# Optimization experiments

Measured on AMD Instinct MI355X. Metric: run time of the kernel, lower is better.

Reference implementation:

```python
import jax, jax.numpy as jnp
import numpy as np

HEADS = 16
DIM_HEAD = 64
SCALE = DIM_HEAD ** -0.5


def setup_inputs() -> dict:
    key = jax.random.key(0)
    k1, k2, k3, k4 = jax.random.split(key, 4)
    b, n, dim = 2, 2048, 1024
    inner = HEADS * DIM_HEAD  # 1024
    x = jax.random.normal(k1, (b, n, dim), dtype=jnp.float32)
    mask = jax.random.randint(k2, (b, n), 0, 2, dtype=jnp.int32)
    Wqkv = jax.random.normal(k3, (dim, inner), dtype=jnp.float32) * (dim ** -0.5)
    Wout = jax.random.normal(k4, (inner, dim), dtype=jnp.float32) * (inner ** -0.5)
    bout = jnp.zeros((dim,), dtype=jnp.float32)
    return {"x": x, "mask": mask, "Wqkv": Wqkv, "Wout": Wout, "bout": bout}


def reference(x, mask, Wqkv, Wout, bout):
    b, n, _ = x.shape
    # shared projection: w acts as q = k = v (CRATE subspace attention)
    w = jnp.einsum('bnd,de->bne', x, Wqkv)
    w = w.reshape(b, n, HEADS, DIM_HEAD).transpose(0, 2, 1, 3)  # b h n d
    dots = jnp.einsum('bhid,bhjd->bhij', w, w) * SCALE           # b h n n
    attn = jax.nn.softmax(dots, axis=-1)
    # post-softmax multiplicative masking (mask=1 zeros the column)
    m = mask[:, None, None, :].astype(attn.dtype)
    attn = attn * (1.0 - m)
    out = jnp.einsum('bhij,bhjd->bhid', attn, w)                 # b h n d
    out = out.transpose(0, 2, 1, 3).reshape(b, n, HEADS * DIM_HEAD)
    return jnp.einsum('bne,ed->bnd', out, Wout) + bout
```

## Files before the change

### kernel.cpp

```cpp
#include <hip/hip_runtime.h>
#include <hip/hip_bf16.h>
#include <stdint.h>

typedef unsigned short u16;
typedef unsigned int u32;
typedef __bf16 bf16x8 __attribute__((ext_vector_type(8)));
typedef float f32x4 __attribute__((ext_vector_type(4)));

#define AS1 __attribute__((address_space(1)))
#define AS3 __attribute__((address_space(3)))

__device__ __forceinline__ void async16(const u16* g, u16* l) {
  __builtin_amdgcn_global_load_lds((const AS1 uint32_t*)(const void*)g,
                                   (AS3 uint32_t*)l, 16, 0, 0);
}

__device__ __forceinline__ u16 f2bf(float v) {
  union { __hip_bfloat16 b; u16 u; } c; c.b = __float2bfloat16(v); return c.u;
}

__device__ __forceinline__ uint4 pack8(float4 lo, float4 hi) {
  uint4 q;
  q.x = (u32)f2bf(lo.x) | ((u32)f2bf(lo.y) << 16);
  q.y = (u32)f2bf(lo.z) | ((u32)f2bf(lo.w) << 16);
  q.z = (u32)f2bf(hi.x) | ((u32)f2bf(hi.y) << 16);
  q.w = (u32)f2bf(hi.z) | ((u32)f2bf(hi.w) << 16);
  return q;
}

__global__ void cvt_x(const float* __restrict__ in, u16* __restrict__ out) {
  int i = (blockIdx.x * 256 + threadIdx.x) * 8;
  float4 lo = *(const float4*)(in + i);
  float4 hi = *(const float4*)(in + i + 4);
  *(uint4*)(out + i) = pack8(lo, hi);
}

__global__ void transpose1024_cvt2(const float* __restrict__ in0, u16* __restrict__ out0,
                                   const float* __restrict__ in1, u16* __restrict__ out1) {
  const float* in = blockIdx.z ? in1 : in0;
  u16* out = blockIdx.z ? out1 : out0;
  __shared__ u16 tile[32][33];
  int tx = threadIdx.x, ty = threadIdx.y;
  int c0 = blockIdx.x * 32, r0 = blockIdx.y * 32;
#pragma unroll
  for (int i = 0; i < 32; i += 8)
    tile[ty + i][tx] = f2bf(in[(size_t)(r0 + ty + i) * 1024 + c0 + tx]);
  __syncthreads();
#pragma unroll
  for (int i = 0; i < 32; i += 8)
    out[(size_t)(c0 + ty + i) * 1024 + r0 + tx] = tile[tx][ty + i];
}

__global__ void scale_transpose_v(const u16* __restrict__ w, const int* __restrict__ mask,
                                  u16* __restrict__ Vt) {
  __shared__ u16 tile[32][33];
  const int tx = threadIdx.x, ty = threadIdx.y;
  const int j0 = blockIdx.x * 32, d0 = blockIdx.y * 32;
  const int bh = blockIdx.z, b = bh >> 4, hc = (bh & 15) * 64;
#pragma unroll
  for (int i = 0; i < 32; i += 8) {
    int j = j0 + ty + i;
    u16 v = w[(size_t)(b * 2048 + j) * 1024 + hc + d0 + tx];
    tile[ty + i][tx] = mask[b * 2048 + j] ? (u16)0 : v;
  }
  __syncthreads();
#pragma unroll
  for (int i = 0; i < 32; i += 8)
    Vt[((size_t)bh * 64 + d0 + ty + i) * 2048 + j0 + tx] = tile[tx][ty + i];
}

template<bool OUT_F32>
__launch_bounds__(256)
__global__ void gemm_bt(const u16* __restrict__ A, const u16* __restrict__ BT,
                        void* __restrict__ Cp, const float* __restrict__ bias,
                        int M, int N, int K) {
  __shared__ __align__(16) u16 As[2][128 * 32];
  __shared__ __align__(16) u16 Bs[2][64 * 32];
  const int t = threadIdx.x;
  const int lane = t & 63, wave = t >> 6;
  const int m0 = blockIdx.x * 128, n0 = blockIdx.y * 64;
  const int wm = (wave & 1) * 64, wn = (wave >> 1) * 32;
  const int lrow = lane & 15, quad = lane >> 4;

  f32x4 acc[4][2] = {};

  const int ar = t >> 2, ac = (t & 3) * 8;
  const u16* gA = A + (size_t)(m0 + ar) * K + ac;
  const u16* gB = BT + (size_t)(n0 + ar) * K + ac;

  for (int k0 = 0; k0 < K; k0 += 64) {
    async16(gA + k0,                       &As[0][t * 8]);
    async16(gA + k0 + (size_t)64 * K,      &As[0][t * 8 + 2048]);
    async16(gA + k0 + 32,                  &As[1][t * 8]);
    async16(gA + k0 + 32 + (size_t)64 * K, &As[1][t * 8 + 2048]);
    async16(gB + k0,                       &Bs[0][t * 8]);
    async16(gB + k0 + 32,                  &Bs[1][t * 8]);
    __syncthreads();

#pragma unroll
    for (int kk = 0; kk < 2; kk++) {
      bf16x8 af[4], bfr[2];
#pragma unroll
      for (int i = 0; i < 4; i++)
        af[i] = *(const bf16x8*)&As[kk][(wm + i * 16 + lrow) * 32 + quad * 8];
#pragma unroll
      for (int j = 0; j < 2; j++)
        bfr[j] = *(const bf16x8*)&Bs[kk][(wn + j * 16 + lrow) * 32 + quad * 8];
#pragma unroll
      for (int i = 0; i < 4; i++)
#pragma unroll
        for (int j = 0; j < 2; j++)
          acc[i][j] = __builtin_amdgcn_mfma_f32_16x16x32_bf16(af[i], bfr[j], acc[i][j], 0, 0, 0);
    }
    __syncthreads();
  }

  float bv[2];
#pragma unroll
  for (int j = 0; j < 2; j++)
    bv[j] = bias ? bias[n0 + wn + j * 16 + lrow] : 0.f;

#pragma unroll
  for (int i = 0; i < 4; i++) {
#pragma unroll
    for (int r = 0; r < 4; r++) {
      int row = m0 + wm + i * 16 + quad * 4 + r;
#pragma unroll
      for (int j = 0; j < 2; j++) {
        size_t ci = (size_t)row * N + n0 + wn + j * 16 + lrow;
        float v = acc[i][j][r] + bv[j];
        if (OUT_F32) ((float*)Cp)[ci] = v;
        else ((u16*)Cp)[ci] = f2bf(v);
      }
    }
  }
}

#define SV 72
#define C1 0.18033688f
#define C2 -28.853901f
__launch_bounds__(256)
__global__ void attn_kernel(const u16* __restrict__ w, const u16* __restrict__ Vt,
                            u16* __restrict__ y) {
  __shared__ __align__(16) u16 Ws[64 * SV];
  __shared__ __align__(16) u16 VTs[64 * SV];
  __shared__ __align__(16) u16 P[4][16 * SV];
  const int t = threadIdx.x, lane = t & 63, wave = t >> 6;
  const int lrow = lane & 15, quad = lane >> 4;
  const int bh = blockIdx.y, b = bh >> 4, h = bh & 15;
  const int q0 = blockIdx.x * 64;
  const size_t rowb = (size_t)b * 2048;
  const int hc = h * 64;
  u16* Pw = P[wave];

  const int sr = t >> 2, sc = (t & 3) * 16;
  const u16* kg = &w[(rowb + sr) * 1024 + hc + sc];
  const u16* vg = &Vt[((size_t)bh * 64 + sr) * 2048 + sc];

  bf16x8 qf0, qf1;
  {
    const size_t qrow = rowb + q0 + wave * 16 + lrow;
    qf0 = *(const bf16x8*)&w[qrow * 1024 + hc + quad * 8];
    qf1 = *(const bf16x8*)&w[qrow * 1024 + hc + 32 + quad * 8];
  }

  uint4 ka = *(const uint4*)kg, kb = *(const uint4*)(kg + 8);
  uint4 va = *(const uint4*)vg, vc = *(const uint4*)(vg + 8);

  f32x4 o[4] = {};
  float lrun[4] = {0.f, 0.f, 0.f, 0.f};

  for (int j0 = 0; j0 < 2048; j0 += 64) {
    __syncthreads();
    *(uint4*)&Ws[sr * SV + sc]      = ka;
    *(uint4*)&Ws[sr * SV + sc + 8]  = kb;
    *(uint4*)&VTs[sr * SV + sc]     = va;
    *(uint4*)&VTs[sr * SV + sc + 8] = vc;
    __syncthreads();

    if (j0 + 64 < 2048) {
      const u16* kn = kg + (size_t)(j0 + 64) * 1024;
      const u16* vn = vg + j0 + 64;
      ka = *(const uint4*)kn; kb = *(const uint4*)(kn + 8);
      va = *(const uint4*)vn; vc = *(const uint4*)(vn + 8);
    }

    f32x4 st[4];
#pragma unroll
    for (int jt = 0; jt < 4; jt++) {
      bf16x8 kf0 = *(const bf16x8*)&Ws[(jt * 16 + lrow) * SV + quad * 8];
      bf16x8 kf1 = *(const bf16x8*)&Ws[(jt * 16 + lrow) * SV + 32 + quad * 8];
      f32x4 z = {};
      z = __builtin_amdgcn_mfma_f32_16x16x32_bf16(qf0, kf0, z, 0, 0, 0);
      z = __builtin_amdgcn_mfma_f32_16x16x32_bf16(qf1, kf1, z, 0, 0, 0);
      st[jt] = z;
    }

#pragma unroll
    for (int jt = 0; jt < 4; jt++) {
#pragma unroll
      for (int r = 0; r < 4; r++) {
        float e = exp2f(fmaf(st[jt][r], C1, C2));
        lrun[r] += e;
        Pw[(quad * 4 + r) * SV + jt * 16 + lrow] = f2bf(e);
      }
    }

    bf16x8 pa0 = *(const bf16x8*)&Pw[lrow * SV + quad * 8];
    bf16x8 pa1 = *(const bf16x8*)&Pw[lrow * SV + 32 + quad * 8];
#pragma unroll
    for (int dt = 0; dt < 4; dt++) {
      bf16x8 vb0 = *(const bf16x8*)&VTs[(dt * 16 + lrow) * SV + quad * 8];
      bf16x8 vb1 = *(const bf16x8*)&VTs[(dt * 16 + lrow) * SV + 32 + quad * 8];
      o[dt] = __builtin_amdgcn_mfma_f32_16x16x32_bf16(pa0, vb0, o[dt], 0, 0, 0);
      o[dt] = __builtin_amdgcn_mfma_f32_16x16x32_bf16(pa1, vb1, o[dt], 0, 0, 0);
    }
  }

#pragma unroll
  for (int r = 0; r < 4; r++) {
    float l = lrun[r];
#pragma unroll
    for (int s = 8; s >= 1; s >>= 1)
      l += __shfl_xor(l, s, 64);
    float inv = 1.f / l;
    const size_t orow = rowb + q0 + wave * 16 + quad * 4 + r;
#pragma unroll
    for (int dt = 0; dt < 4; dt++)
      y[orow * 1024 + hc + dt * 16 + lrow] = f2bf(o[dt][r] * inv);
  }
}

extern "C" void kernel_launch(void* const* d_in, const int* in_sizes, int n_in,
                              void* d_out, int out_size, void* d_ws, size_t ws_size,
                              hipStream_t stream) {
  const float* x    = (const float*)d_in[0];
  const int* mask   = (const int*)d_in[1];
  const float* Wqkv = (const float*)d_in[2];
  const float* Wout = (const float*)d_in[3];
  const float* bout = (const float*)d_in[4];
  float* out = (float*)d_out;

  u16* w     = (u16*)d_ws;
  u16* y     = w + 4096 * 1024;
  u16* WqkvT = y + 4096 * 1024;
  u16* WoutT = WqkvT + 1024 * 1024;
  u16* Vt    = WoutT + 1024 * 1024;
  u16* xb    = y;

  cvt_x<<<2048, 256, 0, stream>>>(x, xb);
  transpose1024_cvt2<<<dim3(32, 32, 2), dim3(32, 8), 0, stream>>>(Wqkv, WqkvT, Wout, WoutT);
  gemm_bt<false><<<dim3(32, 16), 256, 0, stream>>>(xb, WqkvT, w, nullptr, 4096, 1024, 1024);
  scale_transpose_v<<<dim3(64, 2, 32), dim3(32, 8), 0, stream>>>(w, mask, Vt);
  attn_kernel<<<dim3(32, 32), 256, 0, stream>>>(w, Vt, y);
  gemm_bt<true><<<dim3(32, 16), 256, 0, stream>>>(y, WoutT, out, bout, 4096, 1024, 1024);
}
```

Baseline: 193.6 us.

## Fuse V mask-transpose into QKV GEMM epilogue, merge prep kernels, double-buffer GEMMs

Folds the x conversion and both weight transposes into a single prep launch. The masked V transpose is moved into the first GEMM's epilogue, staged through shared memory, so the separate scale_transpose_v kernel and its re-read of w go away. Both GEMMs now double-buffer their shared-memory tiles so the next K-slice load overlaps the current MFMA work. This cuts launches and global traffic, at the cost of twice the LDS per GEMM block, which may lower occupancy.

```diff
diff --git a/kernel.cpp b/kernel.cpp
--- a/kernel.cpp
+++ b/kernel.cpp
@@ -1,6 +1,7 @@
 #include <hip/hip_runtime.h>
 #include <hip/hip_bf16.h>
 #include <stdint.h>
+
 
 typedef unsigned short u16;
 typedef unsigned int u32;
@@ -28,17 +29,21 @@
   return q;
 }
 
-__global__ void cvt_x(const float* __restrict__ in, u16* __restrict__ out) {
-  int i = (blockIdx.x * 256 + threadIdx.x) * 8;
-  float4 lo = *(const float4*)(in + i);
-  float4 hi = *(const float4*)(in + i + 4);
-  *(uint4*)(out + i) = pack8(lo, hi);
-}
-
-__global__ void transpose1024_cvt2(const float* __restrict__ in0, u16* __restrict__ out0,
-                                   const float* __restrict__ in1, u16* __restrict__ out1) {
-  const float* in = blockIdx.z ? in1 : in0;
-  u16* out = blockIdx.z ? out1 : out0;
+__global__ void prep(const float* __restrict__ Wqkv, u16* __restrict__ WqkvT,
+                     const float* __restrict__ Wout, u16* __restrict__ WoutT,
+                     const float* __restrict__ x, u16* __restrict__ xb) {
+  const int z = blockIdx.z;
+  if (z >= 2) {
+    int bid = blockIdx.y * 32 + blockIdx.x;
+    size_t i = (((size_t)(z - 2) * 1024 + bid) * 256
+                + threadIdx.y * 32 + threadIdx.x) * 8;
+    float4 lo = *(const float4*)(x + i);
+    float4 hi = *(const float4*)(x + i + 4);
+    *(uint4*)(xb + i) = pack8(lo, hi);
+    return;
+  }
+  const float* in = z ? Wout : Wqkv;
+  u16* out = z ? WoutT : WqkvT;
   __shared__ u16 tile[32][33];
   int tx = threadIdx.x, ty = threadIdx.y;
   int c0 = blockIdx.x * 32, r0 = blockIdx.y * 32;
@@ -51,31 +56,13 @@
     out[(size_t)(c0 + ty + i) * 1024 + r0 + tx] = tile[tx][ty + i];
 }
 
-__global__ void scale_transpose_v(const u16* __restrict__ w, const int* __restrict__ mask,
-                                  u16* __restrict__ Vt) {
-  __shared__ u16 tile[32][33];
-  const int tx = threadIdx.x, ty = threadIdx.y;
-  const int j0 = blockIdx.x * 32, d0 = blockIdx.y * 32;
-  const int bh = blockIdx.z, b = bh >> 4, hc = (bh & 15) * 64;
-#pragma unroll
-  for (int i = 0; i < 32; i += 8) {
-    int j = j0 + ty + i;
-    u16 v = w[(size_t)(b * 2048 + j) * 1024 + hc + d0 + tx];
-    tile[ty + i][tx] = mask[b * 2048 + j] ? (u16)0 : v;
-  }
-  __syncthreads();
-#pragma unroll
-  for (int i = 0; i < 32; i += 8)
-    Vt[((size_t)bh * 64 + d0 + ty + i) * 2048 + j0 + tx] = tile[tx][ty + i];
-}
-
-template<bool OUT_F32>
 __launch_bounds__(256)
-__global__ void gemm_bt(const u16* __restrict__ A, const u16* __restrict__ BT,
-                        void* __restrict__ Cp, const float* __restrict__ bias,
-                        int M, int N, int K) {
-  __shared__ __align__(16) u16 As[2][128 * 32];
-  __shared__ __align__(16) u16 Bs[2][64 * 32];
+__global__ void gemm1_fused(const u16* __restrict__ A, const u16* __restrict__ BT,
+                            u16* __restrict__ w, const int* __restrict__ mask,
+                            u16* __restrict__ Vt) {
+  const int K = 1024, N = 1024;
+  __shared__ __align__(16) u16 As[2][2][128 * 32];
+  __shared__ __align__(16) u16 Bs[2][2][64 * 32];
   const int t = threadIdx.x;
   const int lane = t & 63, wave = t >> 6;
   const int m0 = blockIdx.x * 128, n0 = blockIdx.y * 64;
@@ -88,24 +75,30 @@
   const u16* gA = A + (size_t)(m0 + ar) * K + ac;
   const u16* gB = BT + (size_t)(n0 + ar) * K + ac;
 
+#define STAGE1(buf, k0)                                              \
+  do {                                                               \
+    async16(gA + (k0),                       &As[buf][0][t * 8]);    \
+    async16(gA + (k0) + (size_t)64 * K,      &As[buf][0][t * 8 + 2048]); \
+    async16(gA + (k0) + 32,                  &As[buf][1][t * 8]);    \
+    async16(gA + (k0) + 32 + (size_t)64 * K, &As[buf][1][t * 8 + 2048]); \
+    async16(gB + (k0),                       &Bs[buf][0][t * 8]);    \
+    async16(gB + (k0) + 32,                  &Bs[buf][1][t * 8]);    \
+  } while (0)
+
+  STAGE1(0, 0);
+  __syncthreads();
+  int p = 0;
   for (int k0 = 0; k0 < K; k0 += 64) {
-    async16(gA + k0,                       &As[0][t * 8]);
-    async16(gA + k0 + (size_t)64 * K,      &As[0][t * 8 + 2048]);
-    async16(gA + k0 + 32,                  &As[1][t * 8]);
-    async16(gA + k0 + 32 + (size_t)64 * K, &As[1][t * 8 + 2048]);
-    async16(gB + k0,                       &Bs[0][t * 8]);
-    async16(gB + k0 + 32,                  &Bs[1][t * 8]);
-    __syncthreads();
-
+    if (k0 + 64 < K) STAGE1(p ^ 1, k0 + 64);
 #pragma unroll
     for (int kk = 0; kk < 2; kk++) {
       bf16x8 af[4], bfr[2];
 #pragma unroll
       for (int i = 0; i < 4; i++)
-        af[i] = *(const bf16x8*)&As[kk][(wm + i * 16 + lrow) * 32 + quad * 8];
+        af[i] = *(const bf16x8*)&As[p][kk][(wm + i * 16 + lrow) * 32 + quad * 8];
 #pragma unroll
       for (int j = 0; j < 2; j++)
-        bfr[j] = *(const bf16x8*)&Bs[kk][(wn + j * 16 + lrow) * 32 + quad * 8];
+        bfr[j] = *(const bf16x8*)&Bs[p][kk][(wn + j * 16 + lrow) * 32 + quad * 8];
 #pragma unroll
       for (int i = 0; i < 4; i++)
 #pragma unroll
@@ -113,27 +106,108 @@
           acc[i][j] = __builtin_amdgcn_mfma_f32_16x16x32_bf16(af[i], bfr[j], acc[i][j], 0, 0, 0);
     }
     __syncthreads();
+    p ^= 1;
+  }
+
+  u16* T = &As[0][0][0];
+#pragma unroll
+  for (int i = 0; i < 4; i++) {
+    int4 mk = *(const int4*)&mask[m0 + wm + i * 16 + quad * 4];
+    int mkk[4] = {mk.x, mk.y, mk.z, mk.w};
+#pragma unroll
+    for (int j2 = 0; j2 < 2; j2++) {
+      union { u16 s[4]; double d; } pk;
+#pragma unroll
+      for (int r = 0; r < 4; r++) {
+        int row = wm + i * 16 + quad * 4 + r;
+        u16 v = f2bf(acc[i][j2][r]);
+        w[(size_t)(m0 + row) * N + n0 + wn + j2 * 16 + lrow] = v;
+        pk.s[r] = mkk[r] ? (u16)0 : v;
+      }
+      int col = wn + j2 * 16 + lrow;
+      *(double*)&T[col * 136 + wm + i * 16 + quad * 4] = pk.d;
+    }
+  }
+  __syncthreads();
+  {
+    const int bq = m0 >> 11, jl0 = m0 & 2047, h = n0 >> 6;
+    u16* vt = Vt + ((size_t)(bq * 16 + h) * 64) * 2048 + jl0;
+    const int dd = t >> 2, cc = (t & 3) * 32;
+#pragma unroll
+    for (int c = 0; c < 4; c++) {
+      uint4 q = *(const uint4*)&T[dd * 136 + cc + c * 8];
+      *(uint4*)&vt[(size_t)dd * 2048 + cc + c * 8] = q;
+    }
+  }
+#undef STAGE1
+}
+
+__launch_bounds__(256)
+__global__ void gemm2(const u16* __restrict__ A, const u16* __restrict__ BT,
+                      float* __restrict__ C, const float* __restrict__ bias) {
+  const int K = 1024, N = 1024;
+  __shared__ __align__(16) u16 As[2][2][128 * 32];
+  __shared__ __align__(16) u16 Bs[2][2][64 * 32];
+  const int t = threadIdx.x;
+  const int lane = t & 63, wave = t >> 6;
+  const int m0 = blockIdx.x * 128, n0 = blockIdx.y * 64;
+  const int wm = (wave & 1) * 64, wn = (wave >> 1) * 32;
+  const int lrow = lane & 15, quad = lane >> 4;
+
+  f32x4 acc[4][2] = {};
+
+  const int ar = t >> 2, ac = (t & 3) * 8;
+  const u16* gA = A + (size_t)(m0 + ar) * K + ac;
+  const u16* gB = BT + (size_t)(n0 + ar) * K + ac;
+
+#define STAGE2(buf, k0)                                              \
+  do {                                                               \
+    async16(gA + (k0),                       &As[buf][0][t * 8]);    \
+    async16(gA + (k0) + (size_t)64 * K,      &As[buf][0][t * 8 + 2048]); \
+    async16(gA + (k0) + 32,                  &As[buf][1][t * 8]);    \
+    async16(gA + (k0) + 32 + (size_t)64 * K, &As[buf][1][t * 8 + 2048]); \
+    async16(gB + (k0),                       &Bs[buf][0][t * 8]);    \
+    async16(gB + (k0) + 32,                  &Bs[buf][1][t * 8]);    \
+  } while (0)
+
+  STAGE2(0, 0);
+  __syncthreads();
+  int p = 0;
+  for (int k0 = 0; k0 < K; k0 += 64) {
+    if (k0 + 64 < K) STAGE2(p ^ 1, k0 + 64);
+#pragma unroll
+    for (int kk = 0; kk < 2; kk++) {
+      bf16x8 af[4], bfr[2];
+#pragma unroll
+      for (int i = 0; i < 4; i++)
+        af[i] = *(const bf16x8*)&As[p][kk][(wm + i * 16 + lrow) * 32 + quad * 8];
+#pragma unroll
+      for (int j = 0; j < 2; j++)
+        bfr[j] = *(const bf16x8*)&Bs[p][kk][(wn + j * 16 + lrow) * 32 + quad * 8];
+#pragma unroll
+      for (int i = 0; i < 4; i++)
+#pragma unroll
+        for (int j = 0; j < 2; j++)
+          acc[i][j] = __builtin_amdgcn_mfma_f32_16x16x32_bf16(af[i], bfr[j], acc[i][j], 0, 0, 0);
+    }
+    __syncthreads();
+    p ^= 1;
   }
 
   float bv[2];
 #pragma unroll
   for (int j = 0; j < 2; j++)
-    bv[j] = bias ? bias[n0 + wn + j * 16 + lrow] : 0.f;
-
-#pragma unroll
-  for (int i = 0; i < 4; i++) {
+    bv[j] = bias[n0 + wn + j * 16 + lrow];
+#pragma unroll
+  for (int i = 0; i < 4; i++)
 #pragma unroll
     for (int r = 0; r < 4; r++) {
       int row = m0 + wm + i * 16 + quad * 4 + r;
 #pragma unroll
-      for (int j = 0; j < 2; j++) {
-        size_t ci = (size_t)row * N + n0 + wn + j * 16 + lrow;
-        float v = acc[i][j][r] + bv[j];
-        if (OUT_F32) ((float*)Cp)[ci] = v;
-        else ((u16*)Cp)[ci] = f2bf(v);
-      }
-    }
-  }
+      for (int j = 0; j < 2; j++)
+        C[(size_t)row * N + n0 + wn + j * 16 + lrow] = acc[i][j][r] + bv[j];
+    }
+#undef STAGE2
 }
 
 #define SV 72
@@ -248,10 +322,8 @@
   u16* Vt    = WoutT + 1024 * 1024;
   u16* xb    = y;
 
-  cvt_x<<<2048, 256, 0, stream>>>(x, xb);
-  transpose1024_cvt2<<<dim3(32, 32, 2), dim3(32, 8), 0, stream>>>(Wqkv, WqkvT, Wout, WoutT);
-  gemm_bt<false><<<dim3(32, 16), 256, 0, stream>>>(xb, WqkvT, w, nullptr, 4096, 1024, 1024);
-  scale_transpose_v<<<dim3(64, 2, 32), dim3(32, 8), 0, stream>>>(w, mask, Vt);
+  prep<<<dim3(32, 32, 4), dim3(32, 8), 0, stream>>>(Wqkv, WqkvT, Wout, WoutT, x, xb);
+  gemm1_fused<<<dim3(32, 16), 256, 0, stream>>>(xb, WqkvT, w, mask, Vt);
   attn_kernel<<<dim3(32, 32), 256, 0, stream>>>(w, Vt, y);
-  gemm_bt<true><<<dim3(32, 16), 256, 0, stream>>>(y, WoutT, out, bout, 4096, 1024, 1024);
-}
+  gemm2<<<dim3(32, 16), 256, 0, stream>>>(y, WoutT, out, bout);
+}
```

Measured after the change: 194.1 us. About the same (+0.3%).
